# Optimization experiments

Measured on AMD Instinct MI355X. Metric: run time of the kernel, lower is better.

The kernel has to match this reference:

```python
import jax, jax.numpy as jnp
import numpy as np


def _knn_gather(x, idx):
    # x: (B,N,D), idx: (B,N,K) -> (B,N,K,D)
    return jax.vmap(lambda xb, ib: xb[ib])(x, idx)


def _frames_and_knn(points, k):
    # brute-force self-KNN (ascending distance; idx[...,0] == self point)
    d2 = jnp.sum(points * points, -1)
    dist = d2[:, :, None] - 2.0 * jnp.einsum('bnd,bmd->bnm', points, points) + d2[:, None, :]
    _, idx = jax.lax.top_k(-dist, k)
    knn = _knn_gather(points, idx)                       # (B,N,K,3)
    cent = knn - knn.mean(-2, keepdims=True)
    # NOTE: original divides by shape[-1]-1 == 2 (coordinate dim), faithful to source
    covs = jnp.einsum('bnki,bnkj->bnij', cent, cent) / 2.0
    _, evecs = jnp.linalg.eigh(covs)
    frames = jnp.swapaxes(evecs, -1, -2)                 # rows = eigvecs, ascending eigval
    det = jnp.linalg.det(frames)                         # det of frames BEFORE modification
    frames = frames.at[:, :, 1, :].multiply(det[..., None])
    return idx, knn, frames


def reference(points, k, local_W):
    B, N, _ = points.shape
    idx, knn, frames = _frames_and_knn(points, k)
    diff = knn - points[:, :, None, :]                   # (B,N,K,3)
    normals = frames[:, :, 0, :]
    t1 = frames[:, :, 1, :]
    t2 = frames[:, :, 2, :]
    dt = jnp.stack([jnp.einsum('bnkd,bnd->bnk', diff, t1),
                    jnp.einsum('bnkd,bnd->bnk', diff, t2)], -1)  # (B,N,K,2)

    # ---- local Voronoi area via tangent-plane grid (nested KNN, K=1) ----
    rescale = 1.1
    bbox_min = dt.min(-2) * rescale                      # (B,N,2)
    bbox_max = dt.max(-2) * rescale
    max_len = (bbox_max - bbox_min).max(-1)              # (B,N)
    coords = (dt - bbox_min[:, :, None, :]) / max_len[:, :, None, None] * 2.0 - 1.0

    lin = jnp.linspace(-1.0, 1.0, local_W, dtype=points.dtype)
    X, Y = jnp.meshgrid(lin, lin, indexing='ij')
    grid = jnp.stack([X, Y], -1).reshape(-1, 2)          # (G,2), G = local_W**2

    CHUNK = 128
    c = coords.reshape(-1, k, 2)
    n_pts = c.shape[0]
    pad = (-n_pts) % CHUNK
    c = jnp.pad(c, ((0, pad), (0, 0), (0, 0)))

    def count_fn(cc):                                    # cc: (CHUNK,K,2)
        d = jnp.sum((grid[None, :, None, :] - cc[:, None, :, :]) ** 2, -1)  # (CHUNK,G,K)
        return jnp.sum(jnp.argmin(d, -1) == 0, -1)       # grid cells owned by center

    counts = jax.lax.map(count_fn, c.reshape(-1, CHUNK, k, 2)).reshape(-1)[:n_pts]
    counts = counts.reshape(B, N).astype(points.dtype)
    voronoi_area = counts * max_len ** 2 / (local_W - 1) ** 2    # (B,N)

    # ---- Weingarten fields / Gaussian curvature ----
    ln = _knn_gather(normals, idx) - normals[:, :, None, :]      # (B,N,K,3)
    dn = jnp.stack([jnp.einsum('bnkd,bnd->bnk', ln, t1),
                    jnp.einsum('bnkd,bnd->bnk', ln, t2)], -1)    # (B,N,K,2)
    XXT = jnp.einsum('bnki,bnkj->bnij', dt, dt)                  # (B,N,2,2)
    YXT = jnp.einsum('bnki,bnkj->bnij', dn, dt)
    S = YXT + jnp.swapaxes(YXT, -1, -2)                          # YXT + XYT
    w, Q = jnp.linalg.eigh(XXT)
    QTSQ = jnp.einsum('bnji,bnjk,bnkl->bnil', Q, S, Q)           # Q^T S Q
    a, b = w[..., 0], w[..., 1]
    cmat = jnp.stack([jnp.stack([2 * a, a + b], -1),
                      jnp.stack([a + b, 2 * b], -1)], -2)        # (B,N,2,2)
    E = QTSQ / (cmat + 1e-8)
    Wmap = jnp.einsum('bnij,bnjk,bnlk->bnil', Q, E, Q)           # Q E Q^T
    gauss = jnp.linalg.det(Wmap)                                 # (B,N)

    euler = jnp.sum(gauss.reshape(-1) * voronoi_area.reshape(-1)) / 2.0 / jnp.pi
    return euler


def setup_inputs() -> dict:
    key = jax.random.key(0)
    points = jax.random.normal(key, (1, 4096, 3), dtype=jnp.float32)
    return {"points": points, "k": 50, "local_W": 64}
```

## Files before the change

kernel.cpp:

```cpp
#include <hip/hip_runtime.h>
#include <math.h>

#define NPTS 4096
#define KNB  50
#define WGRID 64

typedef float v2f __attribute__((ext_vector_type(2)));

__device__ int   g_idx[NPTS * KNB];
__device__ float g_dt[NPTS * KNB * 2];
__device__ float g_nrm[NPTS * 3];
__device__ float g_t1[NPTS * 3];
__device__ float g_t2[NPTS * 3];
__device__ float g_bmin[NPTS * 2];
__device__ float g_ml[NPTS];
__device__ float g_va[NPTS];
__device__ float g_terms[NPTS];

__device__ __forceinline__ float slapy2f(float x, float y) {
  float ax = fabsf(x), ay = fabsf(y);
  float w = fmaxf(ax, ay), z = fminf(ax, ay);
  if (z == 0.0f) return w;
  float t = z / w;
  return w * sqrtf(1.0f + t * t);
}

__device__ __forceinline__ void slartgf(float f, float g, float* cs, float* sn, float* r) {
  const float safmin = 1.1754944e-38f;
  const float safmax = 8.5070592e+37f;
  const float rtmin = 1.0842022e-19f;
  const float rtmax = 6.5219496e+18f;
  if (g == 0.0f) {
    *cs = 1.0f; *sn = 0.0f; *r = f;
  } else if (f == 0.0f) {
    *cs = 0.0f; *sn = copysignf(1.0f, g); *r = fabsf(g);
  } else {
    float f1 = fabsf(f), g1 = fabsf(g);
    if (f1 > rtmin && f1 < rtmax && g1 > rtmin && g1 < rtmax) {
      float d = sqrtf(f * f + g * g);
      float p = 1.0f / d;
      *cs = f1 * p;
      *sn = g * copysignf(p, f);
      *r = copysignf(d, f);
    } else {
      float u = fminf(safmax, fmaxf(safmin, fmaxf(f1, g1)));
      float fs = f / u, gs = g / u;
      float d = sqrtf(fs * fs + gs * gs);
      float p = 1.0f / d;
      *cs = fabsf(fs) * p;
      *sn = gs * copysignf(p, f);
      *r = copysignf(d, f) * u;
    }
  }
}

__device__ void slaev2f(float a, float b, float c, float* rt1, float* rt2,
                        float* cs1, float* sn1) {
  float sm = a + c;
  float df = a - c;
  float adf = fabsf(df);
  float tb = b + b;
  float ab = fabsf(tb);
  float acmx, acmn;
  if (fabsf(a) > fabsf(c)) { acmx = a; acmn = c; } else { acmx = c; acmn = a; }
  float rt;
  if (adf > ab)      { float t = ab / adf; rt = adf * sqrtf(1.0f + t * t); }
  else if (adf < ab) { float t = adf / ab; rt = ab * sqrtf(1.0f + t * t); }
  else               { rt = ab * sqrtf(2.0f); }
  int sgn1;
  if (sm < 0.0f) {
    *rt1 = 0.5f * (sm - rt); sgn1 = -1;
    *rt2 = (acmx / *rt1) * acmn - (b / *rt1) * b;
  } else if (sm > 0.0f) {
    *rt1 = 0.5f * (sm + rt); sgn1 = 1;
    *rt2 = (acmx / *rt1) * acmn - (b / *rt1) * b;
  } else {
    *rt1 = 0.5f * rt; *rt2 = -0.5f * rt; sgn1 = 1;
  }
  float cs; int sgn2;
  if (df >= 0.0f) { cs = df + rt; sgn2 = 1; }
  else            { cs = df - rt; sgn2 = -1; }
  float acs = fabsf(cs);
  if (acs > ab) {
    float ct = -tb / cs;
    *sn1 = 1.0f / sqrtf(1.0f + ct * ct);
    *cs1 = ct * (*sn1);
  } else {
    if (ab == 0.0f) { *cs1 = 1.0f; *sn1 = 0.0f; }
    else {
      float tn = -cs / tb;
      *cs1 = 1.0f / sqrtf(1.0f + tn * tn);
      *sn1 = tn * (*cs1);
    }
  }
  if (sgn1 == sgn2) { float tn = *cs1; *cs1 = -(*sn1); *sn1 = tn; }
}

__device__ void ssteqr3(float* d, float* e, float Z[3][3]) {
  const float eps = 5.9604645e-08f;
  const float eps2 = 3.5527137e-15f;
  const float safmin = 1.1754944e-38f;
  const float ssfmax = 3.0744574e+18f;
  const float ssfmin = 3.0517578e-05f;
  const int n = 3, nmaxit = 90;
  int jtot = 0;
  for (int r = 0; r < 3; ++r)
    for (int c = 0; c < 3; ++c) Z[r][c] = (r == c) ? 1.0f : 0.0f;

  int l1 = 1;
  while (l1 <= n) {
    if (l1 > 1) e[l1 - 2] = 0.0f;
    int m = n;
    for (int mm = l1; mm <= n - 1; ++mm) {
      float tst = fabsf(e[mm - 1]);
      if (tst == 0.0f) { m = mm; break; }
      if (tst <= (sqrtf(fabsf(d[mm - 1])) * sqrtf(fabsf(d[mm]))) * eps) {
        e[mm - 1] = 0.0f; m = mm; break;
      }
    }
    int l = l1, lsv = l1, lend = m, lendsv = m;
    l1 = m + 1;
    if (lend == l) continue;

    float anorm = 0.0f;
    for (int ii = l; ii <= lend; ++ii) anorm = fmaxf(anorm, fabsf(d[ii - 1]));
    for (int ii = l; ii <= lend - 1; ++ii) anorm = fmaxf(anorm, fabsf(e[ii - 1]));
    if (anorm == 0.0f) continue;
    int iscale = 0;
    if (anorm > ssfmax) {
      iscale = 1; float mul = ssfmax / anorm;
      for (int ii = l; ii <= lend; ++ii) d[ii - 1] *= mul;
      for (int ii = l; ii <= lend - 1; ++ii) e[ii - 1] *= mul;
    } else if (anorm < ssfmin) {
      iscale = 2; float mul = ssfmin / anorm;
      for (int ii = l; ii <= lend; ++ii) d[ii - 1] *= mul;
      for (int ii = l; ii <= lend - 1; ++ii) e[ii - 1] *= mul;
    }
    if (fabsf(d[lend - 1]) < fabsf(d[l - 1])) { lend = lsv; l = lendsv; }

    if (lend > l) {
      for (;;) {
        int mm = lend;
        if (l != lend) {
          for (int t = l; t <= lend - 1; ++t) {
            float tst = e[t - 1] * e[t - 1];
            if (tst <= (eps2 * fabsf(d[t - 1])) * fabsf(d[t]) + safmin) { mm = t; break; }
          }
        }
        if (mm < lend) e[mm - 1] = 0.0f;
        float p = d[l - 1];
        if (mm == l) {
          d[l - 1] = p; ++l;
          if (l <= lend) continue; break;
        }
        if (mm == l + 1) {
          float rt1, rt2, c, s;
          slaev2f(d[l - 1], e[l - 1], d[l], &rt1, &rt2, &c, &s);
          for (int r = 0; r < 3; ++r) {
            float t = Z[r][l];
            Z[r][l]     = c * t - s * Z[r][l - 1];
            Z[r][l - 1] = s * t + c * Z[r][l - 1];
          }
          d[l - 1] = rt1; d[l] = rt2; e[l - 1] = 0.0f;
          l += 2;
          if (l <= lend) continue; break;
        }
        if (jtot == nmaxit) break;
        ++jtot;
        float g = (d[l] - p) / (2.0f * e[l - 1]);
        float r = slapy2f(g, 1.0f);
        g = d[mm - 1] - p + e[l - 1] / (g + copysignf(r, g));
        float s = 1.0f, c = 1.0f;
        p = 0.0f;
        float cw[2], sw[2];
        for (int i = mm - 1; i >= l; --i) {
          float f = s * e[i - 1];
          float b = c * e[i - 1];
          slartgf(g, f, &c, &s, &r);
          if (i != mm - 1) e[i] = r;
          g = d[i] - p;
          r = (d[i - 1] - g) * s + 2.0f * c * b;
          p = s * r;
          d[i] = g + p;
          g = c * r - b;
          cw[i - l] = c; sw[i - l] = -s;
        }
        for (int j = mm - 1; j >= l; --j) {
          float cc = cw[j - l], ss = sw[j - l];
          for (int r2 = 0; r2 < 3; ++r2) {
            float t = Z[r2][j];
            Z[r2][j]     = cc * t - ss * Z[r2][j - 1];
            Z[r2][j - 1] = ss * t + cc * Z[r2][j - 1];
          }
        }
        d[l - 1] -= p;
        e[l - 1] = g;
      }
    } else {
      for (;;) {
        int mm = lend;
        if (l != lend) {
          for (int t = l; t >= lend + 1; --t) {
            float tst = e[t - 2] * e[t - 2];
            if (tst <= (eps2 * fabsf(d[t - 1])) * fabsf(d[t - 2]) + safmin) { mm = t; break; }
          }
        }
        if (mm > lend) e[mm - 2] = 0.0f;
        float p = d[l - 1];
        if (mm == l) {
          d[l - 1] = p; --l;
          if (l >= lend) continue; break;
        }
        if (mm == l - 1) {
          float rt1, rt2, c, s;
          slaev2f(d[l - 2], e[l - 2], d[l - 1], &rt1, &rt2, &c, &s);
          for (int r2 = 0; r2 < 3; ++r2) {
            float t = Z[r2][l - 1];
            Z[r2][l - 1] = c * t - s * Z[r2][l - 2];
            Z[r2][l - 2] = s * t + c * Z[r2][l - 2];
          }
          d[l - 2] = rt1; d[l - 1] = rt2; e[l - 2] = 0.0f;
          l -= 2;
          if (l >= lend) continue; break;
        }
        if (jtot == nmaxit) break;
        ++jtot;
        float g = (d[l - 2] - p) / (2.0f * e[l - 2]);
        float r = slapy2f(g, 1.0f);
        g = d[mm - 1] - p + e[l - 2] / (g + copysignf(r, g));
        float s = 1.0f, c = 1.0f;
        p = 0.0f;
        float cw[2], sw[2];
        for (int i = mm; i <= l - 1; ++i) {
          float f = s * e[i - 1];
          float b = c * e[i - 1];
          slartgf(g, f, &c, &s, &r);
          if (i != mm) e[i - 2] = r;
          g = d[i - 1] - p;
          r = (d[i] - g) * s + 2.0f * c * b;
          p = s * r;
          d[i - 1] = g + p;
          g = c * r - b;
          cw[i - mm] = c; sw[i - mm] = s;
        }
        for (int j = mm; j <= l - 1; ++j) {
          float cc = cw[j - mm], ss = sw[j - mm];
          for (int r2 = 0; r2 < 3; ++r2) {
            float t = Z[r2][j];
            Z[r2][j]     = cc * t - ss * Z[r2][j - 1];
            Z[r2][j - 1] = ss * t + cc * Z[r2][j - 1];
          }
        }
        d[l - 1] -= p;
        e[l - 2] = g;
      }
    }
    if (iscale == 1) {
      float mul = anorm / ssfmax;
      for (int ii = lsv; ii <= lendsv; ++ii) d[ii - 1] *= mul;
      for (int ii = lsv; ii <= lendsv - 1; ++ii) e[ii - 1] *= mul;
    } else if (iscale == 2) {
      float mul = anorm / ssfmin;
      for (int ii = lsv; ii <= lendsv; ++ii) d[ii - 1] *= mul;
      for (int ii = lsv; ii <= lendsv - 1; ++ii) e[ii - 1] *= mul;
    }
    if (jtot >= nmaxit) break;
  }
  for (int ii = 2; ii <= n; ++ii) {
    int i0 = ii - 1, k0 = i0;
    float p = d[i0 - 1];
    for (int j = ii; j <= n; ++j)
      if (d[j - 1] < p) { k0 = j; p = d[j - 1]; }
    if (k0 != i0) {
      d[k0 - 1] = d[i0 - 1]; d[i0 - 1] = p;
      for (int r2 = 0; r2 < 3; ++r2) {
        float t = Z[r2][i0 - 1]; Z[r2][i0 - 1] = Z[r2][k0 - 1]; Z[r2][k0 - 1] = t;
      }
    }
  }
}

__device__ void ssytrd3(float a11, float a21, float a31, float a22, float a32, float a33,
                        float d[3], float e[2], float* tau, float* u) {
  float xnorm = fabsf(a31);
  if (xnorm == 0.0f) {
    *tau = 0.0f; *u = 0.0f;
    d[0] = a11; d[1] = a22; d[2] = a33; e[0] = a21; e[1] = a32;
    return;
  }
  float beta = -copysignf(slapy2f(a21, xnorm), a21);
  float taui = (beta - a21) / beta;
  float uu = a31 * (1.0f / (a21 - beta));
  float w1 = taui * a22 + taui * (a32 * uu);
  float w2 = taui * a32 + (taui * uu) * a33;
  float alpha = -0.5f * taui * (w1 + w2 * uu);
  w1 += alpha; w2 += alpha * uu;
  float na22 = a22 - 2.0f * w1;
  float na32 = a32 - (uu * w1 + w2);
  float na33 = a33 - 2.0f * (uu * w2);
  d[0] = a11; d[1] = na22; d[2] = na33;
  e[0] = beta; e[1] = na32;
  *tau = taui; *u = uu;
}

__global__ __launch_bounds__(256) void knn_kernel(const float* __restrict__ pts, int N) {
  __shared__ unsigned skey[NPTS];
  __shared__ unsigned hist[256];
  __shared__ unsigned sred[4];
  __shared__ unsigned sbin[2];
  __shared__ int   eqi[64];
  __shared__ float eqd[64];
  __shared__ unsigned eqn[1];
  const int i = blockIdx.x;
  const int tid = threadIdx.x;
  const int lane = tid & 63, wid = tid >> 6;
  const float xi = pts[3 * i], yi = pts[3 * i + 1], zi = pts[3 * i + 2];
  const float d2i = xi * xi + yi * yi + zi * zi;
  hist[tid] = 0;
  if (tid == 0) eqn[0] = 0;
  __syncthreads();
  for (int j = tid; j < N; j += 256) {
    float xj = pts[3 * j], yj = pts[3 * j + 1], zj = pts[3 * j + 2];
    float d2j = xj * xj + yj * yj + zj * zj;
    float dot = fmaf(zi, zj, fmaf(yi, yj, xi * xj));
    float dist = (d2i - 2.0f * dot) + d2j;
    float dc = fminf(fmaxf(dist, 0.0f), 31.0f);
    unsigned u = (unsigned)(dc * 134217728.0f);
    skey[j] = u;
    atomicAdd(&hist[u >> 24], 1u);
  }
  __syncthreads();
  unsigned prefix = 0, rank = 49;
  for (int pass = 0; pass < 2; ++pass) {
    const int shift = 24 - 8 * pass;
    if (pass) {
      for (int j = tid; j < N; j += 256) {
        unsigned u = skey[j];
        if ((u >> 24) == (prefix >> 24))
          atomicAdd(&hist[(u >> 16) & 255u], 1u);
      }
      __syncthreads();
    }
    unsigned h = hist[tid];
    unsigned c = h;
    #pragma unroll
    for (int off = 1; off < 64; off <<= 1) {
      unsigned o = __shfl_up(c, off);
      if (lane >= off) c += o;
    }
    if (lane == 63) sred[wid] = c;
    __syncthreads();
    unsigned wbase = 0;
    for (int w2 = 0; w2 < wid; ++w2) wbase += sred[w2];
    c += wbase;
    unsigned excl = c - h;
    if (rank >= excl && rank < c) { sbin[0] = (unsigned)tid; sbin[1] = rank - excl; }
    __syncthreads();
    prefix |= sbin[0] << shift;
    rank = sbin[1];
    __syncthreads();
    if (pass == 0) { hist[tid] = 0; __syncthreads(); }
  }
  const unsigned T = prefix;
  int cnt = 0;
  for (int j = tid; j < N; j += 256) {
    unsigned u = skey[j];
    if (u < T && j != i) {
      ++cnt;
    } else if ((u & 0xFFFF0000u) == T) {
      float xj = pts[3 * j], yj = pts[3 * j + 1], zj = pts[3 * j + 2];
      float d2j = xj * xj + yj * yj + zj * zj;
      float dot = fmaf(zi, zj, fmaf(yi, yj, xi * xj));
      float dist = (d2i - 2.0f * dot) + d2j;
      unsigned e = atomicAdd(&eqn[0], 1u);
      if (e < 64u) { eqi[e] = j; eqd[e] = dist; }
    }
  }
  __syncthreads();
  unsigned cc = (unsigned)cnt;
  #pragma unroll
  for (int off = 1; off < 64; off <<= 1) {
    unsigned o = __shfl_up(cc, off);
    if (lane >= off) cc += o;
  }
  if (lane == 63) sred[wid] = cc;
  __syncthreads();
  unsigned wbase = 0;
  for (int w2 = 0; w2 < wid; ++w2) wbase += sred[w2];
  int base = 1 + (int)(wbase + cc - (unsigned)cnt);
  for (int j = tid; j < N; j += 256) {
    unsigned u = skey[j];
    if (u < T && j != i) g_idx[i * KNB + (base++)] = j;
  }
  if (tid == 0) {
    g_idx[i * KNB] = i;
    int slot = 1 + (int)(sred[0] + sred[1] + sred[2] + sred[3]);
    int need = KNB - slot;
    int ne = (int)eqn[0]; if (ne > 64) ne = 64;
    for (int e2 = 0; e2 < need; ++e2) {
      int bq = 0, bidx = 0x7FFFFFFF; float bd = 3.4e38f;
      for (int q = 0; q < ne; ++q) {
        if (eqi[q] < 0) continue;
        float dq = eqd[q];
        if (dq < bd || (dq == bd && eqi[q] < bidx)) { bd = dq; bidx = eqi[q]; bq = q; }
      }
      g_idx[i * KNB + slot + e2] = bidx;
      eqi[bq] = -1;
    }
  }
}

__global__ __launch_bounds__(256) void frames_kernel(const float* __restrict__ pts, int N) {
  __shared__ float sx[4][52], sy[4][52], sz[4][52];
  const int tid = threadIdx.x, lane = tid & 63, w = tid >> 6;
  const int i = blockIdx.x * 4 + w;
  const int base = i * KNB;
  if (lane < KNB) {
    int j = g_idx[base + lane];
    sx[w][lane] = pts[3 * j];
    sy[w][lane] = pts[3 * j + 1];
    sz[w][lane] = pts[3 * j + 2];
  }
  __syncthreads();
  float mx = 0.0f, my = 0.0f, mz = 0.0f;
  for (int kk = 0; kk < KNB; ++kk) { mx += sx[w][kk]; my += sy[w][kk]; mz += sz[w][kk]; }
  mx /= 50.0f; my /= 50.0f; mz /= 50.0f;
  float c00 = 0, c01 = 0, c02 = 0, c11 = 0, c12 = 0, c22 = 0;
  for (int kk = 0; kk < KNB; ++kk) {
    float cx = sx[w][kk] - mx, cy = sy[w][kk] - my, cz = sz[w][kk] - mz;
    c00 = fmaf(cx, cx, c00); c01 = fmaf(cx, cy, c01); c02 = fmaf(cx, cz, c02);
    c11 = fmaf(cy, cy, c11); c12 = fmaf(cy, cz, c12); c22 = fmaf(cz, cz, c22);
  }
  c00 *= 0.5f; c01 *= 0.5f; c02 *= 0.5f; c11 *= 0.5f; c12 *= 0.5f; c22 *= 0.5f;

  float d[3], e[2], tau, u;
  ssytrd3(c00, c01, c02, c11, c12, c22, d, e, &tau, &u);
  float Z[3][3];
  ssteqr3(d, e, Z);
  if (tau != 0.0f) {
    for (int c = 0; c < 3; ++c) {
      float sum = Z[1][c] + u * Z[2][c];
      Z[1][c] -= tau * sum;
      Z[2][c] -= tau * u * sum;
    }
  }
  float n0 = Z[0][0], n1 = Z[1][0], n2 = Z[2][0];
  float a0 = Z[0][1], a1 = Z[1][1], a2 = Z[2][1];
  float b0 = Z[0][2], b1 = Z[1][2], b2 = Z[2][2];
  float cxp = a1 * b2 - a2 * b1, cyp = a2 * b0 - a0 * b2, czp = a0 * b1 - a1 * b0;
  float det = n0 * cxp + n1 * cyp + n2 * czp;
  a0 *= det; a1 *= det; a2 *= det;

  const float xi = pts[3 * i], yi = pts[3 * i + 1], zi = pts[3 * i + 2];
  float dt0 = 0.0f, dt1 = 0.0f;
  float mn0 = 3.0e38f, mx0 = -3.0e38f, mn1 = 3.0e38f, mx1 = -3.0e38f;
  if (lane < KNB) {
    float dx = sx[w][lane] - xi, dy = sy[w][lane] - yi, dz = sz[w][lane] - zi;
    dt0 = dx * a0 + dy * a1 + dz * a2;
    dt1 = dx * b0 + dy * b1 + dz * b2;
    g_dt[2 * (base + lane)] = dt0;
    g_dt[2 * (base + lane) + 1] = dt1;
    mn0 = dt0; mx0 = dt0; mn1 = dt1; mx1 = dt1;
  }
  #pragma unroll
  for (int off = 32; off > 0; off >>= 1) {
    mn0 = fminf(mn0, __shfl_down(mn0, off));
    mx0 = fmaxf(mx0, __shfl_down(mx0, off));
    mn1 = fminf(mn1, __shfl_down(mn1, off));
    mx1 = fmaxf(mx1, __shfl_down(mx1, off));
  }
  if (lane == 0) {
    g_nrm[3 * i] = n0; g_nrm[3 * i + 1] = n1; g_nrm[3 * i + 2] = n2;
    g_t1[3 * i] = a0;  g_t1[3 * i + 1] = a1;  g_t1[3 * i + 2] = a2;
    g_t2[3 * i] = b0;  g_t2[3 * i + 1] = b1;  g_t2[3 * i + 2] = b2;
    float bmin0 = mn0 * 1.1f, bmax0 = mx0 * 1.1f;
    float bmin1 = mn1 * 1.1f, bmax1 = mx1 * 1.1f;
    float ml = fmaxf(bmax0 - bmin0, bmax1 - bmin1);
    g_bmin[2 * i] = bmin0; g_bmin[2 * i + 1] = bmin1;
    g_ml[i] = ml;
  }
}

__global__ __launch_bounds__(512) void voronoi_kernel(int N) {
  __shared__ float2 sc[KNB];
  __shared__ int swc[8];
  const int i = blockIdx.x;
  const int tid = threadIdx.x;
  const int lane = tid & 63, wid = tid >> 6;
  const float ml = g_ml[i];
  const float b0 = g_bmin[2 * i], b1 = g_bmin[2 * i + 1];
  if (tid < KNB) {
    float dt0 = g_dt[2 * (i * KNB + tid)];
    float dt1 = g_dt[2 * (i * KNB + tid) + 1];
    sc[tid] = make_float2((dt0 - b0) / ml * 2.0f - 1.0f,
                          (dt1 - b1) / ml * 2.0f - 1.0f);
  }
  __syncthreads();
  const float step = 2.0f / 63.0f;
  const float gx = fmaf((float)lane, step, -1.0f);
  const float c0x = sc[0].x, c0y = sc[0].y;
  const float ex = gx - c0x;
  v2f gy01, gy23, gy45, gy67;
  gy01.x = fmaf((float)(wid * 8 + 0), step, -1.0f);
  gy01.y = fmaf((float)(wid * 8 + 1), step, -1.0f);
  gy23.x = fmaf((float)(wid * 8 + 2), step, -1.0f);
  gy23.y = fmaf((float)(wid * 8 + 3), step, -1.0f);
  gy45.x = fmaf((float)(wid * 8 + 4), step, -1.0f);
  gy45.y = fmaf((float)(wid * 8 + 5), step, -1.0f);
  gy67.x = fmaf((float)(wid * 8 + 6), step, -1.0f);
  gy67.y = fmaf((float)(wid * 8 + 7), step, -1.0f);
  v2f d001, d023, d045, d067;
#define D0(P) { float eya = gy##P.x - c0y; d0##P.x = ex * ex + eya * eya; \
                float eyb = gy##P.y - c0y; d0##P.y = ex * ex + eyb * eyb; }
  D0(01) D0(23) D0(45) D0(67)
#undef D0
  v2f m01 = {3.0e38f, 3.0e38f}, m23 = {3.0e38f, 3.0e38f};
  v2f m45 = {3.0e38f, 3.0e38f}, m67 = {3.0e38f, 3.0e38f};
  for (int j = 1; j < KNB; ++j) {
    float2 cc = sc[j];
    float dx = gx - cc.x;
    v2f dxv; dxv.x = dx; dxv.y = dx;
    v2f ccy; ccy.x = cc.y; ccy.y = cc.y;
#define VORO_STEP(P) { v2f dy = gy##P - ccy;                                   \
                       v2f dd = __builtin_elementwise_fma(dxv, dxv, dy * dy);  \
                       m##P.x = fminf(m##P.x, dd.x);                           \
                       m##P.y = fminf(m##P.y, dd.y); }
    VORO_STEP(01) VORO_STEP(23) VORO_STEP(45) VORO_STEP(67)
#undef VORO_STEP
    if ((j & 7) == 0) {
      int dead = (m01.x < d001.x) & (m01.y < d001.y)
               & (m23.x < d023.x) & (m23.y < d023.y)
               & (m45.x < d045.x) & (m45.y < d045.y)
               & (m67.x < d067.x) & (m67.y < d067.y);
      if (__all(dead)) break;
    }
  }
  int cnt = 0;
#define VORO_CNT(P) { cnt += (d0##P.x <= m##P.x) ? 1 : 0;                      \
                      cnt += (d0##P.y <= m##P.y) ? 1 : 0; }
  VORO_CNT(01) VORO_CNT(23) VORO_CNT(45) VORO_CNT(67)
#undef VORO_CNT
  #pragma unroll
  for (int off = 32; off > 0; off >>= 1) cnt += __shfl_down(cnt, off);
  if (lane == 0) swc[wid] = cnt;
  __syncthreads();
  if (tid == 0) {
    int tot = 0;
    for (int w2 = 0; w2 < 8; ++w2) tot += swc[w2];
    g_va[i] = (float)tot * (ml * ml) / 3969.0f;
  }
}

__global__ __launch_bounds__(256) void curv_kernel(int N) {
  __shared__ float s0[4][52], s1[4][52], tx[4][52], ty[4][52], tz[4][52];
  const int tid = threadIdx.x, lane = tid & 63, w = tid >> 6;
  const int i = blockIdx.x * 4 + w;
  const int base = i * KNB;
  if (lane < KNB) {
    int j = g_idx[base + lane];
    s0[w][lane] = g_dt[2 * (base + lane)];
    s1[w][lane] = g_dt[2 * (base + lane) + 1];
    tx[w][lane] = g_nrm[3 * j];
    ty[w][lane] = g_nrm[3 * j + 1];
    tz[w][lane] = g_nrm[3 * j + 2];
  }
  __syncthreads();
  float nx = g_nrm[3 * i], ny = g_nrm[3 * i + 1], nz = g_nrm[3 * i + 2];
  float ax = g_t1[3 * i], ay = g_t1[3 * i + 1], az = g_t1[3 * i + 2];
  float bx = g_t2[3 * i], by = g_t2[3 * i + 1], bz = g_t2[3 * i + 2];
  float xx = 0, xy = 0, yy = 0;
  float y00 = 0, y01 = 0, y10 = 0, y11 = 0;
  for (int kk = 0; kk < KNB; ++kk) {
    float dt0 = s0[w][kk], dt1 = s1[w][kk];
    float lx = tx[w][kk] - nx, ly = ty[w][kk] - ny, lz = tz[w][kk] - nz;
    float dn0 = lx * ax + ly * ay + lz * az;
    float dn1 = lx * bx + ly * by + lz * bz;
    xx = fmaf(dt0, dt0, xx); xy = fmaf(dt0, dt1, xy); yy = fmaf(dt1, dt1, yy);
    y00 = fmaf(dn0, dt0, y00); y01 = fmaf(dn0, dt1, y01);
    y10 = fmaf(dn1, dt0, y10); y11 = fmaf(dn1, dt1, y11);
  }
  float s00 = y00 + y00, s01 = y01 + y10, s11 = y11 + y11;
  float rt1, rt2, cs1, sn1;
  slaev2f(xx, xy, yy, &rt1, &rt2, &cs1, &sn1);
  float a, bb, q00, q10, q01, q11;
  if (rt1 <= rt2) { a = rt1; bb = rt2; q00 = cs1; q10 = sn1; q01 = -sn1; q11 = cs1; }
  else            { a = rt2; bb = rt1; q00 = -sn1; q10 = cs1; q01 = cs1; q11 = sn1; }
  float t00 = s00 * q00 + s01 * q10, t01 = s00 * q01 + s01 * q11;
  float t10 = s01 * q00 + s11 * q10, t11 = s01 * q01 + s11 * q11;
  float m00 = q00 * t00 + q10 * t10;
  float m01 = q00 * t01 + q10 * t11;
  float m10 = q01 * t00 + q11 * t10;
  float m11 = q01 * t01 + q11 * t11;
  float e00 = m00 / (2.0f * a + 1e-8f);
  float e01 = m01 / ((a + bb) + 1e-8f);
  float e10 = m10 / ((a + bb) + 1e-8f);
  float e11 = m11 / (2.0f * bb + 1e-8f);
  float u00 = q00 * e00 + q01 * e10, u01 = q00 * e01 + q01 * e11;
  float u10 = q10 * e00 + q11 * e10, u11 = q10 * e01 + q11 * e11;
  float w00 = u00 * q00 + u01 * q01;
  float w01 = u00 * q10 + u01 * q11;
  float w10 = u10 * q00 + u11 * q01;
  float w11 = u10 * q10 + u11 * q11;
  float gauss = w00 * w11 - w01 * w10;
  if (lane == 0) g_terms[i] = gauss * g_va[i];
}

__global__ __launch_bounds__(256) void reduce_kernel(float* __restrict__ out, int N) {
  __shared__ float sw[4];
  float s = 0.0f;
  for (int j = threadIdx.x; j < N; j += 256) s += g_terms[j];
  const int lane = threadIdx.x & 63, wid = threadIdx.x >> 6;
  #pragma unroll
  for (int off = 32; off > 0; off >>= 1) s += __shfl_down(s, off);
  if (lane == 0) sw[wid] = s;
  __syncthreads();
  if (threadIdx.x == 0) {
    float tot = sw[0] + sw[1] + sw[2] + sw[3];
    out[0] = (tot / 2.0f) / 3.14159265358979323846f;
  }
}

extern "C" void kernel_launch(void* const* d_in, const int* in_sizes, int n_in,
                              void* d_out, int out_size, void* d_ws, size_t ws_size,
                              hipStream_t stream) {
  const float* pts = (const float*)d_in[0];
  const int N = in_sizes[0] / 3;
  knn_kernel<<<N, 256, 0, stream>>>(pts, N);
  frames_kernel<<<N / 4, 256, 0, stream>>>(pts, N);
  voronoi_kernel<<<N, 512, 0, stream>>>(N);
  curv_kernel<<<N / 4, 256, 0, stream>>>(N);
  reduce_kernel<<<1, 256, 0, stream>>>((float*)d_out, N);
}
```

Measured before the change: 182.7 us.

## Fuse five kernels into two: knn+frames and voronoi+curvature with atomic reduce

```diff
diff --git a/kernel.cpp b/kernel.cpp
--- a/kernel.cpp
+++ b/kernel.cpp
@@ -14,8 +14,6 @@
 __device__ float g_t2[NPTS * 3];
 __device__ float g_bmin[NPTS * 2];
 __device__ float g_ml[NPTS];
-__device__ float g_va[NPTS];
-__device__ float g_terms[NPTS];
 
 __device__ __forceinline__ float slapy2f(float x, float y) {
   float ax = fabsf(x), ay = fabsf(y);
@@ -303,7 +301,8 @@
   *tau = taui; *u = uu;
 }
 
-__global__ __launch_bounds__(256) void knn_kernel(const float* __restrict__ pts, int N) {
+__global__ __launch_bounds__(256) void knn_frames_kernel(const float* __restrict__ pts,
+                                                         float* __restrict__ out, int N) {
   __shared__ unsigned skey[NPTS];
   __shared__ unsigned hist[256];
   __shared__ unsigned sred[4];
@@ -311,9 +310,12 @@
   __shared__ int   eqi[64];
   __shared__ float eqd[64];
   __shared__ unsigned eqn[1];
+  __shared__ int   sidx[52];
+  __shared__ float sxw[52], syw[52], szw[52];
   const int i = blockIdx.x;
   const int tid = threadIdx.x;
   const int lane = tid & 63, wid = tid >> 6;
+  if (i == 0 && tid == 0) out[0] = 0.0f;
   const float xi = pts[3 * i], yi = pts[3 * i + 1], zi = pts[3 * i + 2];
   const float d2i = xi * xi + yi * yi + zi * zi;
   hist[tid] = 0;
@@ -390,10 +392,10 @@
   int base = 1 + (int)(wbase + cc - (unsigned)cnt);
   for (int j = tid; j < N; j += 256) {
     unsigned u = skey[j];
-    if (u < T && j != i) g_idx[i * KNB + (base++)] = j;
+    if (u < T && j != i) { g_idx[i * KNB + base] = j; sidx[base] = j; ++base; }
   }
   if (tid == 0) {
-    g_idx[i * KNB] = i;
+    g_idx[i * KNB] = i; sidx[0] = i;
     int slot = 1 + (int)(sred[0] + sred[1] + sred[2] + sred[3]);
     int need = KNB - slot;
     int ne = (int)eqn[0]; if (ne > 64) ne = 64;
@@ -404,35 +406,29 @@
         float dq = eqd[q];
         if (dq < bd || (dq == bd && eqi[q] < bidx)) { bd = dq; bidx = eqi[q]; bq = q; }
       }
-      g_idx[i * KNB + slot + e2] = bidx;
+      g_idx[i * KNB + slot + e2] = bidx; sidx[slot + e2] = bidx;
       eqi[bq] = -1;
     }
   }
-}
-
-__global__ __launch_bounds__(256) void frames_kernel(const float* __restrict__ pts, int N) {
-  __shared__ float sx[4][52], sy[4][52], sz[4][52];
-  const int tid = threadIdx.x, lane = tid & 63, w = tid >> 6;
-  const int i = blockIdx.x * 4 + w;
-  const int base = i * KNB;
-  if (lane < KNB) {
-    int j = g_idx[base + lane];
-    sx[w][lane] = pts[3 * j];
-    sy[w][lane] = pts[3 * j + 1];
-    sz[w][lane] = pts[3 * j + 2];
-  }
-  __syncthreads();
+  __syncthreads();
+  if (tid < KNB) {
+    int j = sidx[tid];
+    sxw[tid] = pts[3 * j];
+    syw[tid] = pts[3 * j + 1];
+    szw[tid] = pts[3 * j + 2];
+  }
+  __syncthreads();
+  if (tid >= 64) return;
   float mx = 0.0f, my = 0.0f, mz = 0.0f;
-  for (int kk = 0; kk < KNB; ++kk) { mx += sx[w][kk]; my += sy[w][kk]; mz += sz[w][kk]; }
+  for (int kk = 0; kk < KNB; ++kk) { mx += sxw[kk]; my += syw[kk]; mz += szw[kk]; }
   mx /= 50.0f; my /= 50.0f; mz /= 50.0f;
   float c00 = 0, c01 = 0, c02 = 0, c11 = 0, c12 = 0, c22 = 0;
   for (int kk = 0; kk < KNB; ++kk) {
-    float cx = sx[w][kk] - mx, cy = sy[w][kk] - my, cz = sz[w][kk] - mz;
+    float cx = sxw[kk] - mx, cy = syw[kk] - my, cz = szw[kk] - mz;
     c00 = fmaf(cx, cx, c00); c01 = fmaf(cx, cy, c01); c02 = fmaf(cx, cz, c02);
     c11 = fmaf(cy, cy, c11); c12 = fmaf(cy, cz, c12); c22 = fmaf(cz, cz, c22);
   }
   c00 *= 0.5f; c01 *= 0.5f; c02 *= 0.5f; c11 *= 0.5f; c12 *= 0.5f; c22 *= 0.5f;
-
   float d[3], e[2], tau, u;
   ssytrd3(c00, c01, c02, c11, c12, c22, d, e, &tau, &u);
   float Z[3][3];
@@ -450,16 +446,14 @@
   float cxp = a1 * b2 - a2 * b1, cyp = a2 * b0 - a0 * b2, czp = a0 * b1 - a1 * b0;
   float det = n0 * cxp + n1 * cyp + n2 * czp;
   a0 *= det; a1 *= det; a2 *= det;
-
-  const float xi = pts[3 * i], yi = pts[3 * i + 1], zi = pts[3 * i + 2];
   float dt0 = 0.0f, dt1 = 0.0f;
   float mn0 = 3.0e38f, mx0 = -3.0e38f, mn1 = 3.0e38f, mx1 = -3.0e38f;
   if (lane < KNB) {
-    float dx = sx[w][lane] - xi, dy = sy[w][lane] - yi, dz = sz[w][lane] - zi;
+    float dx = sxw[lane] - xi, dy = syw[lane] - yi, dz = szw[lane] - zi;
     dt0 = dx * a0 + dy * a1 + dz * a2;
     dt1 = dx * b0 + dy * b1 + dz * b2;
-    g_dt[2 * (base + lane)] = dt0;
-    g_dt[2 * (base + lane) + 1] = dt1;
+    g_dt[2 * (i * KNB + lane)] = dt0;
+    g_dt[2 * (i * KNB + lane) + 1] = dt1;
     mn0 = dt0; mx0 = dt0; mn1 = dt1; mx1 = dt1;
   }
   #pragma unroll
@@ -481,46 +475,57 @@
   }
 }
 
-__global__ __launch_bounds__(512) void voronoi_kernel(int N) {
+__global__ __launch_bounds__(512) void voro_curv_kernel(float* __restrict__ out, int N) {
   __shared__ float2 sc[KNB];
   __shared__ int swc[8];
+  __shared__ float sva[1];
+  __shared__ float s0[52], s1[52], txs[52], tys[52], tzs[52];
   const int i = blockIdx.x;
   const int tid = threadIdx.x;
   const int lane = tid & 63, wid = tid >> 6;
   const float ml = g_ml[i];
   const float b0 = g_bmin[2 * i], b1 = g_bmin[2 * i + 1];
   if (tid < KNB) {
+    int j = g_idx[i * KNB + tid];
     float dt0 = g_dt[2 * (i * KNB + tid)];
     float dt1 = g_dt[2 * (i * KNB + tid) + 1];
     sc[tid] = make_float2((dt0 - b0) / ml * 2.0f - 1.0f,
                           (dt1 - b1) / ml * 2.0f - 1.0f);
+    s0[tid] = dt0; s1[tid] = dt1;
+    txs[tid] = g_nrm[3 * j];
+    tys[tid] = g_nrm[3 * j + 1];
+    tzs[tid] = g_nrm[3 * j + 2];
   }
   __syncthreads();
   const float step = 2.0f / 63.0f;
-  const float gx = fmaf((float)lane, step, -1.0f);
+  const int tx = wid & 1, ty = wid >> 1;
+  const int lx = lane & 31, lh = lane >> 5;
+  const int gxi = tx * 32 + lx;
+  const int gyb = ty * 16 + lh * 8;
+  const float gx = fmaf((float)gxi, step, -1.0f);
   const float c0x = sc[0].x, c0y = sc[0].y;
   const float ex = gx - c0x;
   v2f gy01, gy23, gy45, gy67;
-  gy01.x = fmaf((float)(wid * 8 + 0), step, -1.0f);
-  gy01.y = fmaf((float)(wid * 8 + 1), step, -1.0f);
-  gy23.x = fmaf((float)(wid * 8 + 2), step, -1.0f);
-  gy23.y = fmaf((float)(wid * 8 + 3), step, -1.0f);
-  gy45.x = fmaf((float)(wid * 8 + 4), step, -1.0f);
-  gy45.y = fmaf((float)(wid * 8 + 5), step, -1.0f);
-  gy67.x = fmaf((float)(wid * 8 + 6), step, -1.0f);
-  gy67.y = fmaf((float)(wid * 8 + 7), step, -1.0f);
+  gy01.x = fmaf((float)(gyb + 0), step, -1.0f);
+  gy01.y = fmaf((float)(gyb + 1), step, -1.0f);
+  gy23.x = fmaf((float)(gyb + 2), step, -1.0f);
+  gy23.y = fmaf((float)(gyb + 3), step, -1.0f);
+  gy45.x = fmaf((float)(gyb + 4), step, -1.0f);
+  gy45.y = fmaf((float)(gyb + 5), step, -1.0f);
+  gy67.x = fmaf((float)(gyb + 6), step, -1.0f);
+  gy67.y = fmaf((float)(gyb + 7), step, -1.0f);
   v2f d001, d023, d045, d067;
 #define D0(P) { float eya = gy##P.x - c0y; d0##P.x = ex * ex + eya * eya; \
-                float eyb = gy##P.y - c0y; d0##P.y = ex * ex + eyb * eyb; }
+                float eyb2 = gy##P.y - c0y; d0##P.y = ex * ex + eyb2 * eyb2; }
   D0(01) D0(23) D0(45) D0(67)
 #undef D0
   v2f m01 = {3.0e38f, 3.0e38f}, m23 = {3.0e38f, 3.0e38f};
   v2f m45 = {3.0e38f, 3.0e38f}, m67 = {3.0e38f, 3.0e38f};
   for (int j = 1; j < KNB; ++j) {
-    float2 cc = sc[j];
-    float dx = gx - cc.x;
+    float2 ccs = sc[j];
+    float dx = gx - ccs.x;
     v2f dxv; dxv.x = dx; dxv.y = dx;
-    v2f ccy; ccy.x = cc.y; ccy.y = cc.y;
+    v2f ccy; ccy.x = ccs.y; ccy.y = ccs.y;
 #define VORO_STEP(P) { v2f dy = gy##P - ccy;                                   \
                        v2f dd = __builtin_elementwise_fma(dxv, dxv, dy * dy);  \
                        m##P.x = fminf(m##P.x, dd.x);                           \
@@ -547,34 +552,20 @@
   if (tid == 0) {
     int tot = 0;
     for (int w2 = 0; w2 < 8; ++w2) tot += swc[w2];
-    g_va[i] = (float)tot * (ml * ml) / 3969.0f;
-  }
-}
-
-__global__ __launch_bounds__(256) void curv_kernel(int N) {
-  __shared__ float s0[4][52], s1[4][52], tx[4][52], ty[4][52], tz[4][52];
-  const int tid = threadIdx.x, lane = tid & 63, w = tid >> 6;
-  const int i = blockIdx.x * 4 + w;
-  const int base = i * KNB;
-  if (lane < KNB) {
-    int j = g_idx[base + lane];
-    s0[w][lane] = g_dt[2 * (base + lane)];
-    s1[w][lane] = g_dt[2 * (base + lane) + 1];
-    tx[w][lane] = g_nrm[3 * j];
-    ty[w][lane] = g_nrm[3 * j + 1];
-    tz[w][lane] = g_nrm[3 * j + 2];
-  }
-  __syncthreads();
+    sva[0] = (float)tot * (ml * ml) / 3969.0f;
+  }
+  __syncthreads();
+  if (tid >= 64) return;
   float nx = g_nrm[3 * i], ny = g_nrm[3 * i + 1], nz = g_nrm[3 * i + 2];
   float ax = g_t1[3 * i], ay = g_t1[3 * i + 1], az = g_t1[3 * i + 2];
   float bx = g_t2[3 * i], by = g_t2[3 * i + 1], bz = g_t2[3 * i + 2];
   float xx = 0, xy = 0, yy = 0;
   float y00 = 0, y01 = 0, y10 = 0, y11 = 0;
   for (int kk = 0; kk < KNB; ++kk) {
-    float dt0 = s0[w][kk], dt1 = s1[w][kk];
-    float lx = tx[w][kk] - nx, ly = ty[w][kk] - ny, lz = tz[w][kk] - nz;
-    float dn0 = lx * ax + ly * ay + lz * az;
-    float dn1 = lx * bx + ly * by + lz * bz;
+    float dt0 = s0[kk], dt1 = s1[kk];
+    float lxv = txs[kk] - nx, lyv = tys[kk] - ny, lzv = tzs[kk] - nz;
+    float dn0 = lxv * ax + lyv * ay + lzv * az;
+    float dn1 = lxv * bx + lyv * by + lzv * bz;
     xx = fmaf(dt0, dt0, xx); xy = fmaf(dt0, dt1, xy); yy = fmaf(dt1, dt1, yy);
     y00 = fmaf(dn0, dt0, y00); y01 = fmaf(dn0, dt1, y01);
     y10 = fmaf(dn1, dt0, y10); y11 = fmaf(dn1, dt1, y11);
@@ -588,11 +579,11 @@
   float t00 = s00 * q00 + s01 * q10, t01 = s00 * q01 + s01 * q11;
   float t10 = s01 * q00 + s11 * q10, t11 = s01 * q01 + s11 * q11;
   float m00 = q00 * t00 + q10 * t10;
-  float m01 = q00 * t01 + q10 * t11;
+  float m01v = q00 * t01 + q10 * t11;
   float m10 = q01 * t00 + q11 * t10;
   float m11 = q01 * t01 + q11 * t11;
   float e00 = m00 / (2.0f * a + 1e-8f);
-  float e01 = m01 / ((a + bb) + 1e-8f);
+  float e01 = m01v / ((a + bb) + 1e-8f);
   float e10 = m10 / ((a + bb) + 1e-8f);
   float e11 = m11 / (2.0f * bb + 1e-8f);
   float u00 = q00 * e00 + q01 * e10, u01 = q00 * e01 + q01 * e11;
@@ -602,32 +593,16 @@
   float w10 = u10 * q00 + u11 * q01;
   float w11 = u10 * q10 + u11 * q11;
   float gauss = w00 * w11 - w01 * w10;
-  if (lane == 0) g_terms[i] = gauss * g_va[i];
-}
-
-__global__ __launch_bounds__(256) void reduce_kernel(float* __restrict__ out, int N) {
-  __shared__ float sw[4];
-  float s = 0.0f;
-  for (int j = threadIdx.x; j < N; j += 256) s += g_terms[j];
-  const int lane = threadIdx.x & 63, wid = threadIdx.x >> 6;
-  #pragma unroll
-  for (int off = 32; off > 0; off >>= 1) s += __shfl_down(s, off);
-  if (lane == 0) sw[wid] = s;
-  __syncthreads();
-  if (threadIdx.x == 0) {
-    float tot = sw[0] + sw[1] + sw[2] + sw[3];
-    out[0] = (tot / 2.0f) / 3.14159265358979323846f;
-  }
+  if (lane == 0)
+    atomicAdd(out, gauss * sva[0] * 0.15915494309189535f);
 }
 
 extern "C" void kernel_launch(void* const* d_in, const int* in_sizes, int n_in,
                               void* d_out, int out_size, void* d_ws, size_t ws_size,
                               hipStream_t stream) {
   const float* pts = (const float*)d_in[0];
+  float* out = (float*)d_out;
   const int N = in_sizes[0] / 3;
-  knn_kernel<<<N, 256, 0, stream>>>(pts, N);
-  frames_kernel<<<N / 4, 256, 0, stream>>>(pts, N);
-  voronoi_kernel<<<N, 512, 0, stream>>>(N);
-  curv_kernel<<<N / 4, 256, 0, stream>>>(N);
-  reduce_kernel<<<1, 256, 0, stream>>>((float*)d_out, N);
-}
+  knn_frames_kernel<<<N, 256, 0, stream>>>(pts, out, N);
+  voro_curv_kernel<<<N, 512, 0, stream>>>(out, N);
+}
```

Measured after the change: 275.5 us. 1.51x slower.

## Sort Voronoi sites per wave by row distance and fuse final reduction via atomics

Applied to the files above, without the earlier changes.

```diff
diff --git a/kernel.cpp b/kernel.cpp
--- a/kernel.cpp
+++ b/kernel.cpp
@@ -15,7 +15,6 @@
 __device__ float g_bmin[NPTS * 2];
 __device__ float g_ml[NPTS];
 __device__ float g_va[NPTS];
-__device__ float g_terms[NPTS];
 
 __device__ __forceinline__ float slapy2f(float x, float y) {
   float ax = fabsf(x), ay = fabsf(y);
@@ -303,7 +302,8 @@
   *tau = taui; *u = uu;
 }
 
-__global__ __launch_bounds__(256) void knn_kernel(const float* __restrict__ pts, int N) {
+__global__ __launch_bounds__(256) void knn_kernel(const float* __restrict__ pts,
+                                                  float* __restrict__ out, int N) {
   __shared__ unsigned skey[NPTS];
   __shared__ unsigned hist[256];
   __shared__ unsigned sred[4];
@@ -314,6 +314,7 @@
   const int i = blockIdx.x;
   const int tid = threadIdx.x;
   const int lane = tid & 63, wid = tid >> 6;
+  if (i == 0 && tid == 0) out[0] = 0.0f;
   const float xi = pts[3 * i], yi = pts[3 * i + 1], zi = pts[3 * i + 2];
   const float d2i = xi * xi + yi * yi + zi * zi;
   hist[tid] = 0;
@@ -483,6 +484,7 @@
 
 __global__ __launch_bounds__(512) void voronoi_kernel(int N) {
   __shared__ float2 sc[KNB];
+  __shared__ float2 ss[8][49];
   __shared__ int swc[8];
   const int i = blockIdx.x;
   const int tid = threadIdx.x;
@@ -497,6 +499,18 @@
   }
   __syncthreads();
   const float step = 2.0f / 63.0f;
+  const float yc = fmaf((float)(wid * 8) + 3.5f, step, -1.0f);
+  if (lane < 49) {
+    float2 s = sc[lane + 1];
+    float key = fabsf(s.y - yc);
+    int rank = 0;
+    for (int q = 0; q < 49; ++q) {
+      float kq = fabsf(sc[q + 1].y - yc);
+      rank += (kq < key || (kq == key && q < lane)) ? 1 : 0;
+    }
+    ss[wid][rank] = s;
+  }
+  __syncthreads();
   const float gx = fmaf((float)lane, step, -1.0f);
   const float c0x = sc[0].x, c0y = sc[0].y;
   const float ex = gx - c0x;
@@ -511,23 +525,23 @@
   gy67.y = fmaf((float)(wid * 8 + 7), step, -1.0f);
   v2f d001, d023, d045, d067;
 #define D0(P) { float eya = gy##P.x - c0y; d0##P.x = ex * ex + eya * eya; \
-                float eyb = gy##P.y - c0y; d0##P.y = ex * ex + eyb * eyb; }
+                float eyb2 = gy##P.y - c0y; d0##P.y = ex * ex + eyb2 * eyb2; }
   D0(01) D0(23) D0(45) D0(67)
 #undef D0
   v2f m01 = {3.0e38f, 3.0e38f}, m23 = {3.0e38f, 3.0e38f};
   v2f m45 = {3.0e38f, 3.0e38f}, m67 = {3.0e38f, 3.0e38f};
-  for (int j = 1; j < KNB; ++j) {
-    float2 cc = sc[j];
-    float dx = gx - cc.x;
+  for (int j = 0; j < 49; ++j) {
+    float2 ccs = ss[wid][j];
+    float dx = gx - ccs.x;
     v2f dxv; dxv.x = dx; dxv.y = dx;
-    v2f ccy; ccy.x = cc.y; ccy.y = cc.y;
+    v2f ccy; ccy.x = ccs.y; ccy.y = ccs.y;
 #define VORO_STEP(P) { v2f dy = gy##P - ccy;                                   \
                        v2f dd = __builtin_elementwise_fma(dxv, dxv, dy * dy);  \
                        m##P.x = fminf(m##P.x, dd.x);                           \
                        m##P.y = fminf(m##P.y, dd.y); }
     VORO_STEP(01) VORO_STEP(23) VORO_STEP(45) VORO_STEP(67)
 #undef VORO_STEP
-    if ((j & 7) == 0) {
+    if ((j & 3) == 3) {
       int dead = (m01.x < d001.x) & (m01.y < d001.y)
                & (m23.x < d023.x) & (m23.y < d023.y)
                & (m45.x < d045.x) & (m45.y < d045.y)
@@ -551,8 +565,9 @@
   }
 }
 
-__global__ __launch_bounds__(256) void curv_kernel(int N) {
+__global__ __launch_bounds__(256) void curv_kernel(float* __restrict__ out, int N) {
   __shared__ float s0[4][52], s1[4][52], tx[4][52], ty[4][52], tz[4][52];
+  __shared__ float bsum[4];
   const int tid = threadIdx.x, lane = tid & 63, w = tid >> 6;
   const int i = blockIdx.x * 4 + w;
   const int base = i * KNB;
@@ -602,32 +617,20 @@
   float w10 = u10 * q00 + u11 * q01;
   float w11 = u10 * q10 + u11 * q11;
   float gauss = w00 * w11 - w01 * w10;
-  if (lane == 0) g_terms[i] = gauss * g_va[i];
-}
-
-__global__ __launch_bounds__(256) void reduce_kernel(float* __restrict__ out, int N) {
-  __shared__ float sw[4];
-  float s = 0.0f;
-  for (int j = threadIdx.x; j < N; j += 256) s += g_terms[j];
-  const int lane = threadIdx.x & 63, wid = threadIdx.x >> 6;
-  #pragma unroll
-  for (int off = 32; off > 0; off >>= 1) s += __shfl_down(s, off);
-  if (lane == 0) sw[wid] = s;
-  __syncthreads();
-  if (threadIdx.x == 0) {
-    float tot = sw[0] + sw[1] + sw[2] + sw[3];
-    out[0] = (tot / 2.0f) / 3.14159265358979323846f;
-  }
+  if (lane == 0) bsum[w] = gauss * g_va[i] * 0.15915494309189535f;
+  __syncthreads();
+  if (tid == 0)
+    atomicAdd(out, bsum[0] + bsum[1] + bsum[2] + bsum[3]);
 }
 
 extern "C" void kernel_launch(void* const* d_in, const int* in_sizes, int n_in,
                               void* d_out, int out_size, void* d_ws, size_t ws_size,
                               hipStream_t stream) {
   const float* pts = (const float*)d_in[0];
+  float* out = (float*)d_out;
   const int N = in_sizes[0] / 3;
-  knn_kernel<<<N, 256, 0, stream>>>(pts, N);
+  knn_kernel<<<N, 256, 0, stream>>>(pts, out, N);
   frames_kernel<<<N / 4, 256, 0, stream>>>(pts, N);
   voronoi_kernel<<<N, 512, 0, stream>>>(N);
-  curv_kernel<<<N / 4, 256, 0, stream>>>(N);
-  reduce_kernel<<<1, 256, 0, stream>>>((float*)d_out, N);
-}
+  curv_kernel<<<N / 4, 256, 0, stream>>>(out, N);
+}
```

After: 210.9 us. +15.4%, slower.
